# Performance work log

Hardware: AMD Instinct MI355X
Metric: run time of the kernel (lower is better)

The kernel has to match this reference:

```python
import jax, jax.numpy as jnp
import numpy as np
import math

B, S, D, H = 2, 2048, 512, 8
DK = D // H


def setup_inputs() -> dict:
    key = jax.random.key(0)
    ks = jax.random.split(key, 8)
    scale = 1.0 / math.sqrt(D)
    inp = {
        "query": jax.random.normal(ks[0], (B, S, D), dtype=jnp.float32),
        "key": jax.random.normal(ks[1], (B, S, D), dtype=jnp.float32),
        "value": jax.random.normal(ks[2], (B, S, D), dtype=jnp.float32),
        # causal mask, broadcast over batch and heads; masked_fill where mask == 0
        "mask": jnp.tril(jnp.ones((S, S), dtype=jnp.int32))[None, None, :, :],
        # nn.Linear(d_model, d_model, bias=False) weights, shape [out, in]
        "Wq": jax.random.uniform(ks[3], (D, D), jnp.float32, -scale, scale),
        "Wk": jax.random.uniform(ks[4], (D, D), jnp.float32, -scale, scale),
        "Wv": jax.random.uniform(ks[5], (D, D), jnp.float32, -scale, scale),
        "Wo": jax.random.uniform(ks[6], (D, D), jnp.float32, -scale, scale),
    }
    return inp


def reference(query, key, value, mask, Wq, Wk, Wv, Wo):
    b, s, d = query.shape
    h, dk = H, d // H
    q = query @ Wq.T                      # [B,S,D]
    _k_dead = key @ Wk.T                  # computed then discarded by the repo bug
    v = value @ Wv.T                      # [B,S,D]
    # raw .view() head split (NOT transpose-based) — faithful to the source
    qh = q.reshape(b, h, s, dk)           # [B,H,S,dk]
    kh = qh                               # repo bug: key = query.view(...)
    vh = v.reshape(b, h, s, dk)
    scores = jnp.einsum("bhqd,bhkd->bhqk", qh, kh) / math.sqrt(dk)  # [B,H,S,S]
    scores = jnp.where(mask == 0, jnp.float32(-1e9), scores)
    attn = jax.nn.softmax(scores, axis=-1)  # dropout p=0.0 -> identity
    x = jnp.einsum("bhqk,bhkd->bhqd", attn, vh)  # [B,H,S,dk]
    x = x.transpose(0, 2, 1, 3).reshape(b, s, h * dk)  # [B,S,D]
    return x @ Wo.T
```

## Files before the change

### kernel.cpp

```cpp
#include <hip/hip_runtime.h>


typedef unsigned short u16;
typedef unsigned int   u32;
typedef __attribute__((ext_vector_type(4))) float f32x4;
typedef __attribute__((ext_vector_type(8))) short bf16x8;
typedef __attribute__((ext_vector_type(4))) u16   us4;
typedef __attribute__((ext_vector_type(8))) u16   us8;

#define DEV static __device__ __forceinline__

DEV u16 f2b(float x) {
  union { float f; u32 u; } a; a.f = x;
  u32 u = a.u;
  u += 0x7fffu + ((u >> 16) & 1u);
  return (u16)(u >> 16);
}
DEV float b2f(u16 x) { union { u32 u; float f; } a; a.u = (u32)x << 16; return a.f; }
DEV us4 f4tob(f32x4 v) {
  us4 r; r[0] = f2b(v[0]); r[1] = f2b(v[1]); r[2] = f2b(v[2]); r[3] = f2b(v[3]);
  return r;
}

DEV u32 cvtpk(float lo, float hi) {
  u32 d;
  asm("v_cvt_pk_bf16_f32 %0, %1, %2" : "=v"(d) : "v"(lo), "v"(hi));
  return d;
}
DEV void swap32(u32& a, u32& b) {
  asm("v_permlane32_swap_b32 %0, %1" : "+v"(a), "+v"(b));
}
DEV void swap16(u32& a, u32& b) {
  asm("v_permlane16_swap_b32 %0, %1" : "+v"(a), "+v"(b));
}
DEV void swap32f(float& a, float& b) {
  asm("v_permlane32_swap_b32 %0, %1" : "+v"(a), "+v"(b));
}
DEV void swap16f(float& a, float& b) {
  asm("v_permlane16_swap_b32 %0, %1" : "+v"(a), "+v"(b));
}

DEV void gload16(const u16* g, u16* l) {
  __builtin_amdgcn_global_load_lds(
      (const __attribute__((address_space(1))) void*)(const void*)g,
      (__attribute__((address_space(3))) void*)(void*)l, 16, 0, 0);
}

__global__ __launch_bounds__(256)
void cvtw_kernel(const float* __restrict__ wq, const float* __restrict__ wv,
                 const float* __restrict__ wo,
                 u16* __restrict__ bq, u16* __restrict__ bv, u16* __restrict__ bo) {
  int cid = blockIdx.x * 256 + threadIdx.x;
  const float* src; u16* dst; int off;
  if      (cid < 32768) { src = wq; dst = bq; off = cid; }
  else if (cid < 65536) { src = wv; dst = bv; off = cid - 32768; }
  else                  { src = wo; dst = bo; off = cid - 65536; }
  f32x4 a = *reinterpret_cast<const f32x4*>(src + (size_t)off * 8);
  f32x4 b = *reinterpret_cast<const f32x4*>(src + (size_t)off * 8 + 4);
  us4 lo = f4tob(a), hi = f4tob(b);
  us8 o;
  o[0] = lo[0]; o[1] = lo[1]; o[2] = lo[2]; o[3] = lo[3];
  o[4] = hi[0]; o[5] = hi[1]; o[6] = hi[2]; o[7] = hi[3];
  *reinterpret_cast<us8*>(dst + (size_t)off * 8) = o;
}

DEV void ds_writeA(u16* sA, int buf, int tid, const u32 w0[8]) {
  union { u32 wd[4]; us8 v; } o0, o1;
#pragma unroll
  for (int j = 0; j < 4; ++j) { o0.wd[j] = w0[j]; o1.wd[j] = w0[4 + j]; }
  int u0 = 2 * tid;
  int r  = u0 >> 3;
  int s0 = (u0 & 7) ^ (r & 7);
  int s1 = ((u0 + 1) & 7) ^ (r & 7);
  *reinterpret_cast<us8*>(&sA[buf * 4096 + r * 64 + s0 * 8]) = o0.v;
  *reinterpret_cast<us8*>(&sA[buf * 4096 + r * 64 + s1 * 8]) = o1.v;
}

template<int EPI>
DEV void gemm_epilogue(void* outp, int row0, int col0, int wr, int wc,
                       int l16, int lhi, const f32x4 acc[2][2]) {
#pragma unroll
  for (int mf = 0; mf < 2; ++mf)
#pragma unroll
    for (int nf = 0; nf < 2; ++nf)
#pragma unroll
      for (int r = 0; r < 4; ++r) {
        int grow = row0 + wr + mf * 16 + lhi * 4 + r;
        int gcol = col0 + wc + nf * 16 + l16;
        float v = acc[mf][nf][r];
        if constexpr (EPI == 0) {
          ((u16*)outp)[(size_t)grow * 512 + gcol] = f2b(v);
        } else if constexpr (EPI == 1) {
          int b = grow >> 11, srow = grow & 2047;
          int h = srow >> 8;
          int ss = ((srow & 255) << 3) + (gcol >> 6);
          int dd = gcol & 63;
          ((u16*)outp)[(((size_t)(b * 8 + h) * 64 + dd) << 11) + ss] = f2b(v);
        } else {
          ((float*)outp)[(size_t)grow * 512 + gcol] = v;
        }
      }
}

template<int EPI>
DEV void gemm_f32A_body(const float* __restrict__ Af, const u16* __restrict__ Bw,
                        void* __restrict__ outp, int bm, int bn,
                        u16* __restrict__ sA, u16* __restrict__ sB) {
  const int tid  = threadIdx.x;
  const int lane = tid & 63;
  const int w    = tid >> 6;
  const int row0 = bm * 64, col0 = bn * 64;
  const int l16 = lane & 15, lhi = lane >> 4;
  const int wr = (w >> 1) * 32, wc = (w & 1) * 32;
  const int arow = tid >> 2, acol = (tid & 3) * 16;

  f32x4 acc[2][2];
#pragma unroll
  for (int mf = 0; mf < 2; ++mf)
#pragma unroll
    for (int nf = 0; nf < 2; ++nf) acc[mf][nf] = (f32x4)0.f;

  f32x4 ar[4];
  auto loadA = [&](int kt) {
    const float* src = &Af[(size_t)(row0 + arow) * 512 + kt + acol];
#pragma unroll
    for (int j = 0; j < 4; ++j) ar[j] = *reinterpret_cast<const f32x4*>(src + j * 4);
  };
  auto writeA = [&](int buf) {
    u32 wds[8];
#pragma unroll
    for (int j = 0; j < 4; ++j) {
      wds[2 * j]     = cvtpk(ar[j][0], ar[j][1]);
      wds[2 * j + 1] = cvtpk(ar[j][2], ar[j][3]);
    }
    u32 ord[8] = {wds[0], wds[1], wds[2], wds[3], wds[4], wds[5], wds[6], wds[7]};
    ds_writeA(sA, buf, tid, ord);
  };
  auto stageB = [&](int buf, int kt) {
#pragma unroll
    for (int i = 0; i < 2; ++i) {
      int u0 = w * 128 + i * 64;
      int u  = u0 + lane;
      int r  = u >> 3;
      int s  = (u & 7) ^ (r & 7);
      gload16(Bw + (size_t)(col0 + r) * 512 + kt + s * 8, &sB[buf * 4096 + u0 * 8]);
    }
  };

  loadA(0); stageB(0, 0); writeA(0);
  for (int t = 0; t < 8; ++t) {
    __syncthreads();
    if (t + 1 < 8) { stageB((t + 1) & 1, (t + 1) * 64); loadA((t + 1) * 64); }
    const u16* Ka = &sA[(t & 1) * 4096];
    const u16* Kb = &sB[(t & 1) * 4096];
    __builtin_amdgcn_s_setprio(1);
#pragma unroll
    for (int ks = 0; ks < 2; ++ks) {
      bf16x8 af[2], bv[2];
      int unit = (ks * 4 + lhi) ^ (l16 & 7);
#pragma unroll
      for (int mf = 0; mf < 2; ++mf)
        af[mf] = *reinterpret_cast<const bf16x8*>(&Ka[(wr + mf * 16 + l16) * 64 + unit * 8]);
#pragma unroll
      for (int nf = 0; nf < 2; ++nf)
        bv[nf] = *reinterpret_cast<const bf16x8*>(&Kb[(wc + nf * 16 + l16) * 64 + unit * 8]);
#pragma unroll
      for (int mf = 0; mf < 2; ++mf)
#pragma unroll
        for (int nf = 0; nf < 2; ++nf)
          acc[mf][nf] = __builtin_amdgcn_mfma_f32_16x16x32_bf16(af[mf], bv[nf], acc[mf][nf], 0, 0, 0);
    }
    __builtin_amdgcn_s_setprio(0);
    if (t + 1 < 8) writeA((t + 1) & 1);
  }
  gemm_epilogue<EPI>(outp, row0, col0, wr, wc, l16, lhi, acc);
}

__global__ __launch_bounds__(256)
void qv_gemm_kernel(const float* __restrict__ query, const float* __restrict__ value,
                    const u16* __restrict__ wqb, const u16* __restrict__ wvb,
                    u16* __restrict__ qbf, u16* __restrict__ vt) {
  __shared__ u16 sA[2 * 4096];
  __shared__ u16 sB[2 * 4096];
  const int xcd = blockIdx.x & 7;
  const int local = blockIdx.x >> 3;
  const int g = local >> 6, rem = local & 63;
  const int bm = xcd * 8 + (rem >> 3), bn = rem & 7;
  if (g == 0) gemm_f32A_body<0>(query, wqb, qbf, bm, bn, sA, sB);
  else        gemm_f32A_body<1>(value, wvb, vt,  bm, bn, sA, sB);
}

constexpr int NSPLIT = 4;

__global__ __launch_bounds__(256)
void o_gemm_kernel(const u16* __restrict__ opart, const float* __restrict__ lsum,
                   const u16* __restrict__ wob, float* __restrict__ out) {
  __shared__ u16 sA[2 * 4096];
  __shared__ u16 sB[2 * 4096];
  const int tid  = threadIdx.x;
  const int lane = tid & 63;
  const int w    = tid >> 6;
  const int xcd = blockIdx.x & 7;
  const int local = blockIdx.x >> 3;
  const int bm = xcd * 8 + (local >> 3), bn = local & 7;
  const int row0 = bm * 64, col0 = bn * 64;
  const int l16 = lane & 15, lhi = lane >> 4;
  const int wr = (w >> 1) * 32, wc = (w & 1) * 32;
  const int arow = tid >> 2, acol = (tid & 3) * 16;
  const int bb = bm >> 5;
  const int srow = ((bm & 31) << 6) + arow;

  f32x4 acc[2][2];
#pragma unroll
  for (int mf = 0; mf < 2; ++mf)
#pragma unroll
    for (int nf = 0; nf < 2; ++nf) acc[mf][nf] = (f32x4)0.f;

  us8   po[NSPLIT][2];
  float dens[NSPLIT];
  auto loadA = [&](int t) {
    size_t rb = (size_t)(bb * 8 + t) * 2048 + srow;
#pragma unroll
    for (int s = 0; s < NSPLIT; ++s) {
      dens[s] = lsum[(size_t)s * 32768 + rb];
      const u16* src = &opart[((size_t)s * 32768 + rb) * 64 + acol];
      po[s][0] = *reinterpret_cast<const us8*>(src);
      po[s][1] = *reinterpret_cast<const us8*>(src + 8);
    }
  };
  auto writeA = [&](int buf) {
    float inv = 1.f / (dens[0] + dens[1] + dens[2] + dens[3]);
    float a[16];
#pragma unroll
    for (int j = 0; j < 8; ++j) {
      float x0 = 0.f, x1 = 0.f;
#pragma unroll
      for (int s = 0; s < NSPLIT; ++s) {
        x0 += b2f((u16)po[s][0][j]);
        x1 += b2f((u16)po[s][1][j]);
      }
      a[j] = x0 * inv; a[8 + j] = x1 * inv;
    }
    u32 ord[8];
#pragma unroll
    for (int j = 0; j < 8; ++j) ord[j] = cvtpk(a[2 * j], a[2 * j + 1]);
    ds_writeA(sA, buf, tid, ord);
  };
  auto stageB = [&](int buf, int kt) {
#pragma unroll
    for (int i = 0; i < 2; ++i) {
      int u0 = w * 128 + i * 64;
      int u  = u0 + lane;
      int r  = u >> 3;
      int s  = (u & 7) ^ (r & 7);
      gload16(wob + (size_t)(col0 + r) * 512 + kt + s * 8, &sB[buf * 4096 + u0 * 8]);
    }
  };

  loadA(0); stageB(0, 0); writeA(0);
  for (int t = 0; t < 8; ++t) {
    __syncthreads();
    if (t + 1 < 8) { stageB((t + 1) & 1, (t + 1) * 64); loadA(t + 1); }
    const u16* Ka = &sA[(t & 1) * 4096];
    const u16* Kb = &sB[(t & 1) * 4096];
    __builtin_amdgcn_s_setprio(1);
#pragma unroll
    for (int ks = 0; ks < 2; ++ks) {
      bf16x8 af[2], bv[2];
      int unit = (ks * 4 + lhi) ^ (l16 & 7);
#pragma unroll
      for (int mf = 0; mf < 2; ++mf)
        af[mf] = *reinterpret_cast<const bf16x8*>(&Ka[(wr + mf * 16 + l16) * 64 + unit * 8]);
#pragma unroll
      for (int nf = 0; nf < 2; ++nf)
        bv[nf] = *reinterpret_cast<const bf16x8*>(&Kb[(wc + nf * 16 + l16) * 64 + unit * 8]);
#pragma unroll
      for (int mf = 0; mf < 2; ++mf)
#pragma unroll
        for (int nf = 0; nf < 2; ++nf)
          acc[mf][nf] = __builtin_amdgcn_mfma_f32_16x16x32_bf16(af[mf], bv[nf], acc[mf][nf], 0, 0, 0);
    }
    __builtin_amdgcn_s_setprio(0);
    if (t + 1 < 8) writeA((t + 1) & 1);
  }
  gemm_epilogue<2>(out, row0, col0, wr, wc, l16, lhi, acc);
}

constexpr float SCL = 0.125f * 1.44269504088896340736f;

__global__ __launch_bounds__(256)
void attn_kernel(const u16* __restrict__ qbf, const u16* __restrict__ vt,
                 u16* __restrict__ opart, float* __restrict__ lsum) {
  __shared__ u16 sK[2][4096];
  __shared__ u16 sV[2][4096];
  const int tid  = threadIdx.x;
  const int lane = tid & 63;
  const int w    = tid >> 6;
  const int xcd  = blockIdx.x & 7;
  const int i    = blockIdx.x >> 3;
  const int qb   = 31 - (i >> 3);
  const int r8   = i & 7;
  const int bh   = 2 * xcd + (r8 >> 2);
  const int split = r8 & 3;
  const int q0 = qb * 64 + w * 16;
  const int l16 = lane & 15, lhi = lane >> 4;

  const u16* Qh = qbf + (size_t)bh * (2048 * 64);
  const u16* Vh = vt  + (size_t)bh * (64 * 2048);

  bf16x8 qf[2];
#pragma unroll
  for (int ks = 0; ks < 2; ++ks) {
    union { bf16x8 v; u32 wd[4]; } qw;
    qw.v = *reinterpret_cast<const bf16x8*>(&Qh[(q0 + l16) * 64 + ks * 32 + lhi * 8]);
#pragma unroll
    for (int j = 0; j < 4; ++j) {
      u32 u = qw.wd[j];
      float lo = b2f((u16)(u & 0xffffu)) * SCL;
      float hi = b2f((u16)(u >> 16)) * SCL;
      qw.wd[j] = cvtpk(lo, hi);
    }
    qf[ks] = qw.v;
  }

  f32x4 Oa[4];
#pragma unroll
  for (int nf = 0; nf < 4; ++nf) Oa[nf] = (f32x4)0.f;
  float rs = 0.f;

  const int ntiles = qb + 1;
  const int base = ntiles >> 2, rem = ntiles & 3;
  const int t0 = split * base + (split < rem ? split : rem);
  const int t1 = t0 + base + (split < rem ? 1 : 0);

  auto stage = [&](int buf, int t) {
    const int kb = t * 64;
#pragma unroll
    for (int j = 0; j < 2; ++j) {
      int u0 = w * 128 + j * 64;
      int u  = u0 + lane;
      int r  = u >> 3;
      int s  = (u & 7) ^ (r & 7);
      gload16(Qh + (size_t)(kb + r) * 64 + s * 8, &sK[buf][u0 * 8]);
      gload16(Vh + (size_t)r * 2048 + kb + s * 8, &sV[buf][u0 * 8]);
    }
  };

  if (t0 < t1) {
    stage(t0 & 1, t0);
    for (int kt = t0; kt < t1; ++kt) {
      __syncthreads();
      if (kt + 1 < t1) stage((kt + 1) & 1, kt + 1);
      const int kb = kt * 64;
      const u16* Kl = sK[kt & 1];
      const u16* Vl = sV[kt & 1];
      bf16x8 kf[8], vf[8];
#pragma unroll
      for (int nf = 0; nf < 4; ++nf)
#pragma unroll
        for (int ks = 0; ks < 2; ++ks) {
          int off = (nf * 16 + l16) * 64 + (((ks * 4 + lhi) ^ (l16 & 7)) * 8);
          kf[nf * 2 + ks] = *reinterpret_cast<const bf16x8*>(&Kl[off]);
          vf[nf * 2 + ks] = *reinterpret_cast<const bf16x8*>(&Vl[off]);
        }
      f32x4 s[4];
#pragma unroll
      for (int nf = 0; nf < 4; ++nf) s[nf] = (f32x4)0.f;
      __builtin_amdgcn_s_setprio(1);
#pragma unroll
      for (int nf = 0; nf < 4; ++nf)
#pragma unroll
        for (int ks = 0; ks < 2; ++ks)
          s[nf] = __builtin_amdgcn_mfma_f32_16x16x32_bf16(kf[nf * 2 + ks], qf[ks], s[nf], 0, 0, 0);
      __builtin_amdgcn_s_setprio(0);
      if (kb + 63 > q0) {
        const int row = q0 + l16;
#pragma unroll
        for (int nf = 0; nf < 4; ++nf)
#pragma unroll
          for (int r = 0; r < 4; ++r) {
            int col = kb + nf * 16 + lhi * 4 + r;
            if (col > row) s[nf][r] = -1e30f;
          }
      }
#pragma unroll
      for (int nf = 0; nf < 4; ++nf)
#pragma unroll
        for (int r = 0; r < 4; ++r) {
          float p = exp2f(s[nf][r]);
          s[nf][r] = p;
          rs += p;
        }
      u32 pk[4][2];
#pragma unroll
      for (int nf = 0; nf < 4; ++nf)
#pragma unroll
        for (int rr = 0; rr < 2; ++rr)
          pk[nf][rr] = cvtpk(s[nf][2 * rr], s[nf][2 * rr + 1]);
      union { u32 wd[4]; bf16x8 v; } pa[2];
#pragma unroll
      for (int ks = 0; ks < 2; ++ks)
#pragma unroll
        for (int rr = 0; rr < 2; ++rr) {
          u32 X = pk[2 * ks][rr], Y = pk[2 * ks + 1][rr];
          swap32(X, Y);
          swap16(X, Y);
          pa[ks].wd[rr]     = X;
          pa[ks].wd[2 + rr] = Y;
        }
      __builtin_amdgcn_s_setprio(1);
#pragma unroll
      for (int nf = 0; nf < 4; ++nf)
#pragma unroll
        for (int ks = 0; ks < 2; ++ks)
          Oa[nf] = __builtin_amdgcn_mfma_f32_16x16x32_bf16(pa[ks].v, vf[nf * 2 + ks], Oa[nf], 0, 0, 0);
      __builtin_amdgcn_s_setprio(0);
    }
  }

  {
    float a = rs, b = rs;
    swap16f(a, b);
    float y = a + b;
    float c = y, d = y;
    swap32f(c, d);
    rs = c + d;
  }

  u16* op = opart + ((size_t)split * 32768 + bh * 2048) * 64;
#pragma unroll
  for (int nf = 0; nf < 4; ++nf)
#pragma unroll
    for (int r = 0; r < 4; ++r) {
      int row = q0 + lhi * 4 + r;
      op[(size_t)row * 64 + nf * 16 + l16] = f2b(Oa[nf][r]);
    }
  if (lane < 16)
    lsum[(size_t)split * 32768 + bh * 2048 + q0 + lane] = rs;
}

extern "C" void kernel_launch(void* const* d_in, const int* in_sizes, int n_in,
                              void* d_out, int out_size, void* d_ws, size_t ws_size,
                              hipStream_t stream) {
  const float* query = (const float*)d_in[0];
  const float* value = (const float*)d_in[2];
  const float* Wq = (const float*)d_in[4];
  const float* Wv = (const float*)d_in[6];
  const float* Wo = (const float*)d_in[7];

  u16* qbf   = (u16*)d_ws;
  u16* vt    = qbf + 2097152;
  u16* opart = vt + 2097152;
  u16* wqb   = opart + NSPLIT * 2097152;
  u16* wvb   = wqb + 262144;
  u16* wob   = wvb + 262144;
  float* lsum = (float*)(wob + 262144);
  float* out = (float*)d_out;

  cvtw_kernel<<<dim3(384), dim3(256), 0, stream>>>(Wq, Wv, Wo, wqb, wvb, wob);
  qv_gemm_kernel<<<dim3(1024), dim3(256), 0, stream>>>(query, value, wqb, wvb, qbf, vt);
  attn_kernel<<<dim3(2048), dim3(256), 0, stream>>>(qbf, vt, opart, lsum);
  o_gemm_kernel<<<dim3(512), dim3(256), 0, stream>>>(opart, lsum, wob, out);
}
```

Baseline: 67.16 us.

## Split split-K attention merge out of output GEMM into separate kernel

```diff
diff --git a/kernel.cpp b/kernel.cpp
--- a/kernel.cpp
+++ b/kernel.cpp
@@ -127,13 +127,12 @@
     for (int j = 0; j < 4; ++j) ar[j] = *reinterpret_cast<const f32x4*>(src + j * 4);
   };
   auto writeA = [&](int buf) {
-    u32 wds[8];
+    u32 ord[8];
 #pragma unroll
     for (int j = 0; j < 4; ++j) {
-      wds[2 * j]     = cvtpk(ar[j][0], ar[j][1]);
-      wds[2 * j + 1] = cvtpk(ar[j][2], ar[j][3]);
-    }
-    u32 ord[8] = {wds[0], wds[1], wds[2], wds[3], wds[4], wds[5], wds[6], wds[7]};
+      ord[2 * j]     = cvtpk(ar[j][0], ar[j][1]);
+      ord[2 * j + 1] = cvtpk(ar[j][2], ar[j][3]);
+    }
     ds_writeA(sA, buf, tid, ord);
   };
   auto stageB = [&](int buf, int kt) {
@@ -190,11 +189,9 @@
   else        gemm_f32A_body<1>(value, wvb, vt,  bm, bn, sA, sB);
 }
 
-constexpr int NSPLIT = 4;
-
 __global__ __launch_bounds__(256)
-void o_gemm_kernel(const u16* __restrict__ opart, const float* __restrict__ lsum,
-                   const u16* __restrict__ wob, float* __restrict__ out) {
+void o_gemm_kernel(const u16* __restrict__ opre, const u16* __restrict__ wob,
+                   float* __restrict__ out) {
   __shared__ u16 sA[2 * 4096];
   __shared__ u16 sB[2 * 4096];
   const int tid  = threadIdx.x;
@@ -206,9 +203,6 @@
   const int row0 = bm * 64, col0 = bn * 64;
   const int l16 = lane & 15, lhi = lane >> 4;
   const int wr = (w >> 1) * 32, wc = (w & 1) * 32;
-  const int arow = tid >> 2, acol = (tid & 3) * 16;
-  const int bb = bm >> 5;
-  const int srow = ((bm & 31) << 6) + arow;
 
   f32x4 acc[2][2];
 #pragma unroll
@@ -216,51 +210,22 @@
 #pragma unroll
     for (int nf = 0; nf < 2; ++nf) acc[mf][nf] = (f32x4)0.f;
 
-  us8   po[NSPLIT][2];
-  float dens[NSPLIT];
-  auto loadA = [&](int t) {
-    size_t rb = (size_t)(bb * 8 + t) * 2048 + srow;
-#pragma unroll
-    for (int s = 0; s < NSPLIT; ++s) {
-      dens[s] = lsum[(size_t)s * 32768 + rb];
-      const u16* src = &opart[((size_t)s * 32768 + rb) * 64 + acol];
-      po[s][0] = *reinterpret_cast<const us8*>(src);
-      po[s][1] = *reinterpret_cast<const us8*>(src + 8);
-    }
-  };
-  auto writeA = [&](int buf) {
-    float inv = 1.f / (dens[0] + dens[1] + dens[2] + dens[3]);
-    float a[16];
-#pragma unroll
-    for (int j = 0; j < 8; ++j) {
-      float x0 = 0.f, x1 = 0.f;
-#pragma unroll
-      for (int s = 0; s < NSPLIT; ++s) {
-        x0 += b2f((u16)po[s][0][j]);
-        x1 += b2f((u16)po[s][1][j]);
-      }
-      a[j] = x0 * inv; a[8 + j] = x1 * inv;
-    }
-    u32 ord[8];
-#pragma unroll
-    for (int j = 0; j < 8; ++j) ord[j] = cvtpk(a[2 * j], a[2 * j + 1]);
-    ds_writeA(sA, buf, tid, ord);
-  };
-  auto stageB = [&](int buf, int kt) {
+  auto stage = [&](int buf, int kt) {
 #pragma unroll
     for (int i = 0; i < 2; ++i) {
       int u0 = w * 128 + i * 64;
       int u  = u0 + lane;
       int r  = u >> 3;
       int s  = (u & 7) ^ (r & 7);
-      gload16(wob + (size_t)(col0 + r) * 512 + kt + s * 8, &sB[buf * 4096 + u0 * 8]);
+      gload16(opre + (size_t)(row0 + r) * 512 + kt + s * 8, &sA[buf * 4096 + u0 * 8]);
+      gload16(wob  + (size_t)(col0 + r) * 512 + kt + s * 8, &sB[buf * 4096 + u0 * 8]);
     }
   };
 
-  loadA(0); stageB(0, 0); writeA(0);
+  stage(0, 0);
   for (int t = 0; t < 8; ++t) {
     __syncthreads();
-    if (t + 1 < 8) { stageB((t + 1) & 1, (t + 1) * 64); loadA(t + 1); }
+    if (t + 1 < 8) stage((t + 1) & 1, (t + 1) * 64);
     const u16* Ka = &sA[(t & 1) * 4096];
     const u16* Kb = &sB[(t & 1) * 4096];
     __builtin_amdgcn_s_setprio(1);
@@ -281,12 +246,12 @@
           acc[mf][nf] = __builtin_amdgcn_mfma_f32_16x16x32_bf16(af[mf], bv[nf], acc[mf][nf], 0, 0, 0);
     }
     __builtin_amdgcn_s_setprio(0);
-    if (t + 1 < 8) writeA((t + 1) & 1);
   }
   gemm_epilogue<2>(out, row0, col0, wr, wc, l16, lhi, acc);
 }
 
 constexpr float SCL = 0.125f * 1.44269504088896340736f;
+constexpr int NSPLIT = 4;
 
 __global__ __launch_bounds__(256)
 void attn_kernel(const u16* __restrict__ qbf, const u16* __restrict__ vt,
@@ -439,6 +404,33 @@
     lsum[(size_t)split * 32768 + bh * 2048 + q0 + lane] = rs;
 }
 
+__global__ __launch_bounds__(256)
+void merge_kernel(const u16* __restrict__ opart, const float* __restrict__ lsum,
+                  u16* __restrict__ opre) {
+  const int gid = blockIdx.x * 256 + threadIdx.x;
+  const int row = gid >> 3;
+  const int c   = gid & 7;
+  float den = 0.f;
+#pragma unroll
+  for (int s = 0; s < NSPLIT; ++s) den += lsum[(size_t)s * 32768 + row];
+  const float inv = 1.f / den;
+  float acc[8];
+#pragma unroll
+  for (int j = 0; j < 8; ++j) acc[j] = 0.f;
+#pragma unroll
+  for (int s = 0; s < NSPLIT; ++s) {
+    us8 o = *reinterpret_cast<const us8*>(&opart[((size_t)s * 32768 + row) * 64 + c * 8]);
+#pragma unroll
+    for (int j = 0; j < 8; ++j) acc[j] += b2f(o[j]);
+  }
+  us8 o;
+#pragma unroll
+  for (int j = 0; j < 8; ++j) o[j] = f2b(acc[j] * inv);
+  const int bh = row >> 11, srow = row & 2047;
+  const int b = bh >> 3, h = bh & 7;
+  *reinterpret_cast<us8*>(&opre[((size_t)b * 2048 + srow) * 512 + h * 64 + c * 8]) = o;
+}
+
 extern "C" void kernel_launch(void* const* d_in, const int* in_sizes, int n_in,
                               void* d_out, int out_size, void* d_ws, size_t ws_size,
                               hipStream_t stream) {
@@ -450,7 +442,8 @@
 
   u16* qbf   = (u16*)d_ws;
   u16* vt    = qbf + 2097152;
-  u16* opart = vt + 2097152;
+  u16* opre  = vt + 2097152;
+  u16* opart = opre + 2097152;
   u16* wqb   = opart + NSPLIT * 2097152;
   u16* wvb   = wqb + 262144;
   u16* wob   = wvb + 262144;
@@ -460,5 +453,6 @@
   cvtw_kernel<<<dim3(384), dim3(256), 0, stream>>>(Wq, Wv, Wo, wqb, wvb, wob);
   qv_gemm_kernel<<<dim3(1024), dim3(256), 0, stream>>>(query, value, wqb, wvb, qbf, vt);
   attn_kernel<<<dim3(2048), dim3(256), 0, stream>>>(qbf, vt, opart, lsum);
-  o_gemm_kernel<<<dim3(512), dim3(256), 0, stream>>>(opart, lsum, wob, out);
-}
+  merge_kernel<<<dim3(1024), dim3(256), 0, stream>>>(opart, lsum, opre);
+  o_gemm_kernel<<<dim3(512), dim3(256), 0, stream>>>(opre, wob, out);
+}
```

Measured after the change: 66.33 us. No clear change (-1.2%).
